# Kernel tuning notes

Measured on AMD Instinct MI355X. Metric: run time of the kernel, lower is better.

## Reference

```python
import jax, jax.numpy as jnp
import numpy as np
import math

B, S, H = 2, 4096, 512
NUM_HEADS = 8
HEAD_DIM = H // NUM_HEADS
RECENCY_DECAY = 0.9


def setup_inputs() -> dict:
    key = jax.random.key(0)
    k1, k2, k3 = jax.random.split(key, 3)
    scale = 1.0 / math.sqrt(H)
    x = jax.random.normal(k1, (B, S, H), dtype=jnp.float32)
    w_qkv = jax.random.normal(k2, (3 * H, H), dtype=jnp.float32) * scale
    w_out = jax.random.normal(k3, (H, H), dtype=jnp.float32) * scale
    b_out = jnp.zeros((H,), dtype=jnp.float32)
    return {"x": x, "w_qkv": w_qkv, "w_out": w_out, "b_out": b_out}


def reference(x, w_qkv, w_out, b_out):
    batch, seq_len, hidden = x.shape
    nh, hd = NUM_HEADS, HEAD_DIM
    # qkv projection (no bias): torch Linear computes x @ W.T
    qkv = jnp.einsum('bsh,oh->bso', x, w_qkv)
    qkv = qkv.reshape(batch, seq_len, 3, nh, hd)
    q, k, v = jnp.transpose(qkv, (2, 0, 3, 1, 4))  # each [B, nh, S, hd]
    attn = jnp.einsum('bhqd,bhkd->bhqk', q, k) / math.sqrt(hd)
    # recency bias: positions[i, j] = j - i; bias = (j-i)*log(decay) for j<=i else 0
    pos = jnp.arange(seq_len)[None, :] - jnp.arange(seq_len)[:, None]
    bias = jnp.where(pos <= 0, pos.astype(jnp.float32) * math.log(RECENCY_DECAY),
                     jnp.zeros((), dtype=jnp.float32))
    attn = jax.nn.softmax(attn + bias[None, None, :, :], axis=-1)
    out = jnp.einsum('bhqk,bhkd->bqhd', attn, v).reshape(batch, seq_len, hidden)
    return jnp.einsum('bsh,oh->bso', out, w_out) + b_out
```

## Files before the change

### kernel.cpp

```cpp
#include <hip/hip_runtime.h>
#include <hip/hip_bf16.h>
#include <hip/hip_fp16.h>
#include <stdint.h>

#define B_   2
#define S_   4096
#define H_   512
#define NH_  8
#define HD_  64
#define M_   (B_*S_)
#define LOG2D (-0.15200309344504997f)
#define SC2   (0.18033688011112042f)

#define NFULL        4
#define NCHUNK       8

typedef __attribute__((ext_vector_type(8))) short bf16x8_t;
typedef __attribute__((ext_vector_type(4))) float f32x4_t;

__device__ __forceinline__ void gl_lds16(const __hip_bfloat16* g, __hip_bfloat16* l) {
  __builtin_amdgcn_global_load_lds(
      (__attribute__((address_space(1))) void*)(g),
      (__attribute__((address_space(3))) void*)(l),
      16, 0, 0);
}

__global__ __launch_bounds__(256)
void cast3_kernel(const float* __restrict__ x, const float* __restrict__ wq,
                  const float* __restrict__ wo,
                  __hip_bfloat16* __restrict__ xb, __hip_bfloat16* __restrict__ wqb,
                  __hip_bfloat16* __restrict__ wob) {
  const int N0 = M_ * H_;
  const int N1 = 3 * H_ * H_;
  int i4 = (blockIdx.x * blockDim.x + threadIdx.x) * 4;
  const float* src; __hip_bfloat16* dst; int off;
  if (i4 < N0)           { src = x;  dst = xb;  off = i4; }
  else if (i4 < N0 + N1) { src = wq; dst = wqb; off = i4 - N0; }
  else                   { src = wo; dst = wob; off = i4 - N0 - N1; }
  float4 v = *(const float4*)(src + off);
  ushort4 o;
  __hip_bfloat16 h;
  h = __float2bfloat16(v.x); o.x = *(unsigned short*)&h;
  h = __float2bfloat16(v.y); o.y = *(unsigned short*)&h;
  h = __float2bfloat16(v.z); o.z = *(unsigned short*)&h;
  h = __float2bfloat16(v.w); o.w = *(unsigned short*)&h;
  *(ushort4*)((unsigned short*)dst + off) = o;
}

template<int EPI>
__global__ __launch_bounds__(256)
void gemm_bt(const __hip_bfloat16* __restrict__ A,
             const __hip_bfloat16* __restrict__ Bw,
             int K,
             __hip_bfloat16* __restrict__ qb,
             __hip_bfloat16* __restrict__ kb,
             __hip_bfloat16* __restrict__ vtb,
             float* __restrict__ outp,
             const float* __restrict__ bias) {
  __shared__ alignas(16) __hip_bfloat16 sA[128*64];
  __shared__ alignas(16) __hip_bfloat16 sB[128*64];
  const int tid  = threadIdx.x;
  const int wave = tid >> 6, lane = tid & 63;
  const int quad = lane >> 4, l15 = lane & 15;
  const int wr = (wave >> 1) * 64, wc = (wave & 1) * 64;

  const int nbx  = gridDim.x;
  const int flat = blockIdx.y * nbx + blockIdx.x;
  const int xcd  = flat & 7, sq = flat >> 3;
  const int rows_per_xcd = gridDim.y >> 3;
  const int by = xcd * rows_per_xcd + sq / nbx;
  const int bx = sq % nbx;
  const int m0 = by * 128, n0 = bx * 128;

  const int sub  = lane >> 3;
  const int plog = (lane & 7) ^ sub;

  f32x4_t acc[4][4] = {};

  for (int kt = 0; kt < K; kt += 64) {
    __syncthreads();
    #pragma unroll
    for (int cc = 0; cc < 4; cc++) {
      int c   = wave * 4 + cc;
      int row = c * 8 + sub;
      gl_lds16(A  + (size_t)(m0 + row) * K + kt + plog * 8, sA + c * 512);
      gl_lds16(Bw + (size_t)(n0 + row) * K + kt + plog * 8, sB + c * 512);
    }
    __syncthreads();
    #pragma unroll
    for (int kh = 0; kh < 2; kh++) {
      bf16x8_t af[4], bfr[4];
      #pragma unroll
      for (int x = 0; x < 4; x++) {
        int row = wr + x * 16 + l15;
        int pos = kh * 4 + quad;
        af[x] = *(const bf16x8_t*)(sA + row * 64 + ((pos ^ (row & 7)) << 3));
      }
      #pragma unroll
      for (int y = 0; y < 4; y++) {
        int row = wc + y * 16 + l15;
        int pos = kh * 4 + quad;
        bfr[y] = *(const bf16x8_t*)(sB + row * 64 + ((pos ^ (row & 7)) << 3));
      }
      #pragma unroll
      for (int x = 0; x < 4; x++)
        #pragma unroll
        for (int y = 0; y < 4; y++)
          acc[x][y] = __builtin_amdgcn_mfma_f32_16x16x32_bf16(af[x], bfr[y], acc[x][y], 0, 0, 0);
    }
  }

  if (EPI == 0 && (n0 >> 9) == 2) {
    #pragma unroll
    for (int x = 0; x < 4; x++) {
      int gr = m0 + wr + x * 16 + quad * 4;
      int bb = gr >> 12, sb = gr & 4095;
      #pragma unroll
      for (int y = 0; y < 4; y++) {
        int rem = (n0 - 1024) + wc + y * 16 + l15;
        int h = rem >> 6, d = rem & 63;
        ushort4 o; __hip_bfloat16 hv;
        hv = __float2bfloat16(acc[x][y][0]); o.x = *(unsigned short*)&hv;
        hv = __float2bfloat16(acc[x][y][1]); o.y = *(unsigned short*)&hv;
        hv = __float2bfloat16(acc[x][y][2]); o.z = *(unsigned short*)&hv;
        hv = __float2bfloat16(acc[x][y][3]); o.w = *(unsigned short*)&hv;
        *(ushort4*)(vtb + ((size_t)(bb * NH_ + h) * HD_ + d) * S_ + sb) = o;
      }
    }
  } else {
    #pragma unroll
    for (int x = 0; x < 4; x++) {
      #pragma unroll
      for (int y = 0; y < 4; y++) {
        #pragma unroll
        for (int r = 0; r < 4; r++) {
          int gr = m0 + wr + x*16 + quad*4 + r;
          int gc = n0 + wc + y*16 + l15;
          float v = acc[x][y][r];
          if (EPI == 0) {
            int bb = gr >> 12, s = gr & 4095;
            int t  = gc >> 9,  rem = gc & 511;
            int h  = rem >> 6, d = rem & 63;
            __hip_bfloat16 hv = __float2bfloat16(v);
            int bh = bb * NH_ + h;
            if (t == 0) qb[((size_t)bh * S_ + s) * HD_ + d] = hv;
            else        kb[((size_t)bh * S_ + s) * HD_ + d] = hv;
          } else {
            outp[(size_t)gr * H_ + gc] = v + bias[gc];
          }
        }
      }
    }
  }
}

__global__ __launch_bounds__(256)
void gemm_out64(const __hip_bfloat16* __restrict__ A,
                const __hip_bfloat16* __restrict__ Bw,
                float* __restrict__ outp,
                const float* __restrict__ bias) {
  __shared__ alignas(16) __hip_bfloat16 sA[64*64];
  __shared__ alignas(16) __hip_bfloat16 sB[128*64];
  const int tid  = threadIdx.x;
  const int wave = tid >> 6, lane = tid & 63;
  const int quad = lane >> 4, l15 = lane & 15;
  const int wr = (wave >> 1) * 32, wc = (wave & 1) * 64;

  const int flat = blockIdx.x;
  const int xcd  = flat & 7, sq = flat >> 3;
  const int by = xcd * 16 + (sq >> 2);
  const int bx = sq & 3;
  const int m0 = by * 64, n0 = bx * 128;

  const int sub  = lane >> 3;
  const int plog = (lane & 7) ^ sub;

  f32x4_t acc[2][4] = {};

  for (int kt = 0; kt < H_; kt += 64) {
    __syncthreads();
    #pragma unroll
    for (int cc = 0; cc < 6; cc++) {
      int cid = wave * 6 + cc;
      if (cid < 8) {
        int row = cid * 8 + sub;
        gl_lds16(A  + (size_t)(m0 + row) * H_ + kt + plog * 8, sA + cid * 512);
      } else {
        int row = (cid - 8) * 8 + sub;
        gl_lds16(Bw + (size_t)(n0 + row) * H_ + kt + plog * 8, sB + (cid - 8) * 512);
      }
    }
    __syncthreads();
    #pragma unroll
    for (int kh = 0; kh < 2; kh++) {
      bf16x8_t af[2], bfr[4];
      #pragma unroll
      for (int x = 0; x < 2; x++) {
        int row = wr + x * 16 + l15;
        int pos = kh * 4 + quad;
        af[x] = *(const bf16x8_t*)(sA + row * 64 + ((pos ^ (row & 7)) << 3));
      }
      #pragma unroll
      for (int y = 0; y < 4; y++) {
        int row = wc + y * 16 + l15;
        int pos = kh * 4 + quad;
        bfr[y] = *(const bf16x8_t*)(sB + row * 64 + ((pos ^ (row & 7)) << 3));
      }
      #pragma unroll
      for (int x = 0; x < 2; x++)
        #pragma unroll
        for (int y = 0; y < 4; y++)
          acc[x][y] = __builtin_amdgcn_mfma_f32_16x16x32_bf16(af[x], bfr[y], acc[x][y], 0, 0, 0);
    }
  }

  #pragma unroll
  for (int x = 0; x < 2; x++) {
    #pragma unroll
    for (int y = 0; y < 4; y++) {
      #pragma unroll
      for (int r = 0; r < 4; r++) {
        int gr = m0 + wr + x*16 + quad*4 + r;
        int gc = n0 + wc + y*16 + l15;
        outp[(size_t)gr * H_ + gc] = acc[x][y][r] + bias[gc];
      }
    }
  }
}

__device__ __forceinline__ void stage_kv(const __hip_bfloat16* __restrict__ kb,
                                         const __hip_bfloat16* __restrict__ vtb,
                                         int bh, int j0,
                                         __hip_bfloat16* dK, __hip_bfloat16* dV,
                                         int wave, int lane, int sub, int plog) {
  if (wave < 2) {
    #pragma unroll
    for (int cc = 0; cc < 4; cc++) {
      int c = wave * 4 + cc;
      gl_lds16(kb + ((size_t)bh * S_ + j0 + c * 8 + sub) * HD_ + plog * 8, dK + c * 512);
    }
  } else {
    #pragma unroll
    for (int cc = 0; cc < 4; cc++) {
      int c = (wave - 2) * 4 + cc;
      gl_lds16(vtb + ((size_t)bh * HD_ + c * 8 + sub) * S_ + j0 + plog * 8, dV + c * 512);
    }
  }
}

__global__ __launch_bounds__(256)
void attn_kernel(const __hip_bfloat16* __restrict__ qb,
                 const __hip_bfloat16* __restrict__ kb,
                 const __hip_bfloat16* __restrict__ vtb,
                 __hip_bfloat16* __restrict__ ob,
                 __half* __restrict__ pO,
                 float* __restrict__ pl) {
  __shared__ alignas(16) __hip_bfloat16 sK[2][64*64];
  __shared__ alignas(16) __hip_bfloat16 sV[2][64*64];
  __shared__ alignas(16) __hip_bfloat16 sP[4][16*64];

  const int tid  = threadIdx.x;
  const int wave = tid >> 6, lane = tid & 63;
  const int quad = lane >> 4, l15 = lane & 15;

  const int flat = blockIdx.x;
  const int xcd  = flat & 7;
  const int idx  = flat >> 3;
  const int b1   = idx / 92;
  const int w    = idx % 92;
  const int bh   = xcd + (b1 << 3);

  int q0, jt0, niter, chunk = 0;
  bool direct;
  if (w < 60) { q0 = 256 + w * 64; jt0 = 0; niter = 4; direct = true; }
  else { int t = w - 60; chunk = t & 7; q0 = (t >> 3) * 64; jt0 = chunk * 8; niter = 8; direct = false; }

  const __hip_bfloat16* qrow = qb + ((size_t)bh * S_ + q0 + wave * 16 + l15) * HD_;
  bf16x8_t aQ0 = *(const bf16x8_t*)(qrow + quad * 8);
  bf16x8_t aQ1 = *(const bf16x8_t*)(qrow + 32 + quad * 8);

  f32x4_t accO[4] = {};
  float l_r[4], negM2[4];
  const int row_i = q0 + wave * 16 + quad * 4;
  #pragma unroll
  for (int r = 0; r < 4; r++) {
    l_r[r] = 0.f;
    negM2[r] = -(17.312340f - LOG2D * (float)(row_i + r));
  }

  const int sub  = lane >> 3;
  const int plog = (lane & 7) ^ sub;
  __hip_bfloat16* sPw = &sP[wave][0];

  stage_kv(kb, vtb, bh, jt0 * 64, &sK[0][0], &sV[0][0], wave, lane, sub, plog);

  for (int it = 0; it < niter; ++it) {
    const int cur = it & 1;
    __syncthreads();
    if (it < niter - 1)
      stage_kv(kb, vtb, bh, (jt0 + it + 1) * 64,
               &sK[1 - cur][0], &sV[1 - cur][0], wave, lane, sub, plog);
    const __hip_bfloat16* cK = &sK[cur][0];
    const __hip_bfloat16* cV = &sV[cur][0];
    const int j0 = (jt0 + it) * 64;

    f32x4_t sfr[4];
    __builtin_amdgcn_s_setprio(1);
    #pragma unroll
    for (int ni = 0; ni < 4; ni++) {
      int row = ni * 16 + l15;
      f32x4_t a = {};
      bf16x8_t b0 = *(const bf16x8_t*)(cK + row * 64 + ((quad       ^ (row & 7)) << 3));
      bf16x8_t b1v = *(const bf16x8_t*)(cK + row * 64 + (((quad + 4) ^ (row & 7)) << 3));
      a = __builtin_amdgcn_mfma_f32_16x16x32_bf16(aQ0, b0, a, 0, 0, 0);
      a = __builtin_amdgcn_mfma_f32_16x16x32_bf16(aQ1, b1v, a, 0, 0, 0);
      sfr[ni] = a;
    }
    __builtin_amdgcn_s_setprio(0);

    #pragma unroll
    for (int r = 0; r < 4; r++) {
      const float d0 = (float)(j0 + l15 - (row_i + r));
      const int row = quad * 4 + r;
      float psum = 0.f;
      #pragma unroll
      for (int ni = 0; ni < 4; ni++) {
        float dij = d0 + (float)(ni * 16);
        float arg = fmaf(fminf(dij, 0.f), LOG2D, fmaf(sfr[ni][r], SC2, negM2[r]));
        float p = __builtin_amdgcn_exp2f(arg);
        psum += p;
        int col = ni * 16 + l15;
        sPw[row * 64 + (((col >> 3) ^ (row & 7)) << 3) + (col & 7)] = __float2bfloat16(p);
      }
      l_r[r] += psum;
    }
    __builtin_amdgcn_sched_barrier(0);
    __builtin_amdgcn_s_waitcnt(0xC07F);
    __builtin_amdgcn_sched_barrier(0);

    bf16x8_t aP0 = *(const bf16x8_t*)(sPw + l15 * 64 + ((quad       ^ (l15 & 7)) << 3));
    bf16x8_t aP1 = *(const bf16x8_t*)(sPw + l15 * 64 + (((quad + 4) ^ (l15 & 7)) << 3));
    __builtin_amdgcn_s_setprio(1);
    #pragma unroll
    for (int nd = 0; nd < 4; nd++) {
      int row = nd * 16 + l15;
      bf16x8_t b0 = *(const bf16x8_t*)(cV + row * 64 + ((quad       ^ (row & 7)) << 3));
      bf16x8_t b1v = *(const bf16x8_t*)(cV + row * 64 + (((quad + 4) ^ (row & 7)) << 3));
      accO[nd] = __builtin_amdgcn_mfma_f32_16x16x32_bf16(aP0, b0, accO[nd], 0, 0, 0);
      accO[nd] = __builtin_amdgcn_mfma_f32_16x16x32_bf16(aP1, b1v, accO[nd], 0, 0, 0);
    }
    __builtin_amdgcn_s_setprio(0);
    __builtin_amdgcn_sched_barrier(0);
  }

  #pragma unroll
  for (int r = 0; r < 4; r++) {
    float l = l_r[r];
    #pragma unroll
    for (int msk = 1; msk < 16; msk <<= 1) l += __shfl_xor(l, msk, 64);
    l_r[r] = l;
  }

  if (direct) {
    const int b = bh >> 3, h = bh & 7;
    #pragma unroll
    for (int r = 0; r < 4; r++) {
      float invr = 1.0f / l_r[r];
      #pragma unroll
      for (int nd = 0; nd < 4; nd++) {
        int srow = q0 + wave * 16 + quad * 4 + r;
        int col  = h * HD_ + nd * 16 + l15;
        ob[((size_t)b * S_ + srow) * H_ + col] = __float2bfloat16(accO[nd][r] * invr);
      }
    }
  } else {
    const int qt = q0 >> 6;
    size_t base = ((size_t)bh * NFULL + qt) * NCHUNK + chunk;
    __half* po = pO + base * 4096;
    #pragma unroll
    for (int nd = 0; nd < 4; nd++)
      #pragma unroll
      for (int r = 0; r < 4; r++)
        po[(wave*16 + quad*4 + r) * 64 + nd*16 + l15] = __float2half(accO[nd][r]);
    if (l15 == 0) {
      #pragma unroll
      for (int r = 0; r < 4; r++)
        pl[base * 64 + wave*16 + quad*4 + r] = l_r[r];
    }
  }
}

__global__ __launch_bounds__(256)
void combine_kernel(const __half* __restrict__ pO,
                    const float* __restrict__ pl,
                    __hip_bfloat16* __restrict__ ob) {
  const int f  = blockIdx.x;
  const int bh = blockIdx.y;
  const int tid = threadIdx.x;
  const int rr = tid >> 2, cg = (tid & 3) * 16;
  const size_t base0 = ((size_t)bh * NFULL + f) * NCHUNK;

  float L = 0.f;
  #pragma unroll
  for (int c = 0; c < NCHUNK; c++) L += pl[(base0 + c) * 64 + rr];
  const float inv = 1.0f / L;

  float o[16];
  #pragma unroll
  for (int k = 0; k < 16; k++) o[k] = 0.f;
  #pragma unroll
  for (int c = 0; c < NCHUNK; c++) {
    const __half* src = pO + (base0 + c) * 4096 + rr * 64 + cg;
    #pragma unroll
    for (int k = 0; k < 16; k++) o[k] += __half2float(src[k]);
  }
  const int b = bh >> 3, h = bh & 7, s = f * 64 + rr;
  __hip_bfloat16* dst = ob + ((size_t)b * S_ + s) * H_ + h * HD_ + cg;
  #pragma unroll
  for (int k = 0; k < 16; k++) dst[k] = __float2bfloat16(o[k] * inv);
}

extern "C" void kernel_launch(void* const* d_in, const int* in_sizes, int n_in,
                              void* d_out, int out_size, void* d_ws, size_t ws_size,
                              hipStream_t stream) {
  const float* x     = (const float*)d_in[0];
  const float* w_qkv = (const float*)d_in[1];
  const float* w_out = (const float*)d_in[2];
  const float* b_out = (const float*)d_in[3];
  float* out = (float*)d_out;

  char* ws = (char*)d_ws;
  __hip_bfloat16* xb  = (__hip_bfloat16*)(ws);
  __hip_bfloat16* wqb = (__hip_bfloat16*)(ws + (8u  << 20));
  __hip_bfloat16* wob = (__hip_bfloat16*)(ws + (10u << 20));
  __hip_bfloat16* qb  = (__hip_bfloat16*)(ws + (11u << 20));
  __hip_bfloat16* kb  = (__hip_bfloat16*)(ws + (19u << 20));
  __hip_bfloat16* vtb = (__hip_bfloat16*)(ws + (27u << 20));
  __half*         pO  = (__half*)(ws + (36u << 20));
  float*          pl  = (float*)(ws + (41u << 20));
  __hip_bfloat16* ab  = xb;

  cast3_kernel<<<dim3(5120), dim3(256), 0, stream>>>(x, w_qkv, w_out, xb, wqb, wob);
  gemm_bt<0><<<dim3(12, 64), dim3(256), 0, stream>>>(xb, wqb, H_, qb, kb, vtb, nullptr, nullptr);
  attn_kernel<<<dim3(1472), dim3(256), 0, stream>>>(qb, kb, vtb, ab, pO, pl);
  combine_kernel<<<dim3(NFULL, B_ * NH_), dim3(256), 0, stream>>>(pO, pl, ab);
  gemm_out64<<<dim3(512), dim3(256), 0, stream>>>(ab, wob, out, b_out);
}
```

Measured before the change: 134.3 us.

## Process two query tiles per block in direct attention path to reuse K/V tiles

Direct-path attention blocks now each handle two 64-row query tiles (128 rows) and share each staged K/V tile between them, which halves the number of direct blocks and the grid size. The aim is to cut repeated K/V global loads and LDS staging and to spread per-block setup over more work. The cost is more registers for the doubled accumulators and Q fragments, which may lower occupancy, plus fewer blocks to fill the GPU.

```diff
diff --git a/kernel.cpp b/kernel.cpp
--- a/kernel.cpp
+++ b/kernel.cpp
@@ -266,27 +266,37 @@
   const int flat = blockIdx.x;
   const int xcd  = flat & 7;
   const int idx  = flat >> 3;
-  const int b1   = idx / 92;
-  const int w    = idx % 92;
+  const int b1   = idx / 62;
+  const int w    = idx % 62;
   const int bh   = xcd + (b1 << 3);
 
-  int q0, jt0, niter, chunk = 0;
+  int q0, jt0, niter, chunk = 0, NQ;
   bool direct;
-  if (w < 60) { q0 = 256 + w * 64; jt0 = 0; niter = 4; direct = true; }
-  else { int t = w - 60; chunk = t & 7; q0 = (t >> 3) * 64; jt0 = chunk * 8; niter = 8; direct = false; }
-
-  const __hip_bfloat16* qrow = qb + ((size_t)bh * S_ + q0 + wave * 16 + l15) * HD_;
-  bf16x8_t aQ0 = *(const bf16x8_t*)(qrow + quad * 8);
-  bf16x8_t aQ1 = *(const bf16x8_t*)(qrow + 32 + quad * 8);
-
-  f32x4_t accO[4] = {};
-  float l_r[4], negM2[4];
+  if (w < 30) { q0 = 256 + w * 128; jt0 = 0; niter = 4; direct = true;  NQ = 2; }
+  else { int t = w - 30; chunk = t & 7; q0 = (t >> 3) * 64; jt0 = chunk * 8;
+         niter = 8; direct = false; NQ = 1; }
+
+  bf16x8_t aQ0[2], aQ1[2];
+  #pragma unroll
+  for (int qi = 0; qi < 2; qi++) {
+    if (qi < NQ) {
+      const __hip_bfloat16* qrow =
+          qb + ((size_t)bh * S_ + q0 + qi * 64 + wave * 16 + l15) * HD_;
+      aQ0[qi] = *(const bf16x8_t*)(qrow + quad * 8);
+      aQ1[qi] = *(const bf16x8_t*)(qrow + 32 + quad * 8);
+    }
+  }
+
+  f32x4_t accO[2][4] = {};
+  float l_r[2][4], negM2[2][4];
   const int row_i = q0 + wave * 16 + quad * 4;
   #pragma unroll
-  for (int r = 0; r < 4; r++) {
-    l_r[r] = 0.f;
-    negM2[r] = -(17.312340f - LOG2D * (float)(row_i + r));
-  }
+  for (int qi = 0; qi < 2; qi++)
+    #pragma unroll
+    for (int r = 0; r < 4; r++) {
+      l_r[qi][r] = 0.f;
+      negM2[qi][r] = -(17.312340f - LOG2D * (float)(row_i + qi * 64 + r));
+    }
 
   const int sub  = lane >> 3;
   const int plog = (lane & 7) ^ sub;
@@ -304,73 +314,85 @@
     const __hip_bfloat16* cV = &sV[cur][0];
     const int j0 = (jt0 + it) * 64;
 
-    f32x4_t sfr[4];
-    __builtin_amdgcn_s_setprio(1);
-    #pragma unroll
-    for (int ni = 0; ni < 4; ni++) {
-      int row = ni * 16 + l15;
-      f32x4_t a = {};
-      bf16x8_t b0 = *(const bf16x8_t*)(cK + row * 64 + ((quad       ^ (row & 7)) << 3));
-      bf16x8_t b1v = *(const bf16x8_t*)(cK + row * 64 + (((quad + 4) ^ (row & 7)) << 3));
-      a = __builtin_amdgcn_mfma_f32_16x16x32_bf16(aQ0, b0, a, 0, 0, 0);
-      a = __builtin_amdgcn_mfma_f32_16x16x32_bf16(aQ1, b1v, a, 0, 0, 0);
-      sfr[ni] = a;
-    }
-    __builtin_amdgcn_s_setprio(0);
-
+    #pragma unroll
+    for (int qi = 0; qi < 2; qi++) {
+      if (qi >= NQ) break;
+
+      f32x4_t sfr[4];
+      __builtin_amdgcn_s_setprio(1);
+      #pragma unroll
+      for (int ni = 0; ni < 4; ni++) {
+        int row = ni * 16 + l15;
+        f32x4_t a = {};
+        bf16x8_t b0 = *(const bf16x8_t*)(cK + row * 64 + ((quad       ^ (row & 7)) << 3));
+        bf16x8_t b1v = *(const bf16x8_t*)(cK + row * 64 + (((quad + 4) ^ (row & 7)) << 3));
+        a = __builtin_amdgcn_mfma_f32_16x16x32_bf16(aQ0[qi], b0, a, 0, 0, 0);
+        a = __builtin_amdgcn_mfma_f32_16x16x32_bf16(aQ1[qi], b1v, a, 0, 0, 0);
+        sfr[ni] = a;
+      }
+      __builtin_amdgcn_s_setprio(0);
+
+      #pragma unroll
+      for (int r = 0; r < 4; r++) {
+        const float d0 = (float)(j0 + l15 - (row_i + qi * 64 + r));
+        const int row = quad * 4 + r;
+        float psum = 0.f;
+        #pragma unroll
+        for (int ni = 0; ni < 4; ni++) {
+          float dij = d0 + (float)(ni * 16);
+          float arg = fmaf(fminf(dij, 0.f), LOG2D, fmaf(sfr[ni][r], SC2, negM2[qi][r]));
+          float p = __builtin_amdgcn_exp2f(arg);
+          psum += p;
+          int col = ni * 16 + l15;
+          sPw[row * 64 + (((col >> 3) ^ (row & 7)) << 3) + (col & 7)] = __float2bfloat16(p);
+        }
+        l_r[qi][r] += psum;
+      }
+      __builtin_amdgcn_sched_barrier(0);
+      __builtin_amdgcn_s_waitcnt(0xC07F);
+      __builtin_amdgcn_sched_barrier(0);
+
+      bf16x8_t aP0 = *(const bf16x8_t*)(sPw + l15 * 64 + ((quad       ^ (l15 & 7)) << 3));
+      bf16x8_t aP1 = *(const bf16x8_t*)(sPw + l15 * 64 + (((quad + 4) ^ (l15 & 7)) << 3));
+      __builtin_amdgcn_s_setprio(1);
+      #pragma unroll
+      for (int nd = 0; nd < 4; nd++) {
+        int row = nd * 16 + l15;
+        bf16x8_t b0 = *(const bf16x8_t*)(cV + row * 64 + ((quad       ^ (row & 7)) << 3));
+        bf16x8_t b1v = *(const bf16x8_t*)(cV + row * 64 + (((quad + 4) ^ (row & 7)) << 3));
+        accO[qi][nd] = __builtin_amdgcn_mfma_f32_16x16x32_bf16(aP0, b0, accO[qi][nd], 0, 0, 0);
+        accO[qi][nd] = __builtin_amdgcn_mfma_f32_16x16x32_bf16(aP1, b1v, accO[qi][nd], 0, 0, 0);
+      }
+      __builtin_amdgcn_s_setprio(0);
+      __builtin_amdgcn_sched_barrier(0);
+    }
+  }
+
+  #pragma unroll
+  for (int qi = 0; qi < 2; qi++) {
+    if (qi >= NQ) break;
     #pragma unroll
     for (int r = 0; r < 4; r++) {
-      const float d0 = (float)(j0 + l15 - (row_i + r));
-      const int row = quad * 4 + r;
-      float psum = 0.f;
-      #pragma unroll
-      for (int ni = 0; ni < 4; ni++) {
-        float dij = d0 + (float)(ni * 16);
-        float arg = fmaf(fminf(dij, 0.f), LOG2D, fmaf(sfr[ni][r], SC2, negM2[r]));
-        float p = __builtin_amdgcn_exp2f(arg);
-        psum += p;
-        int col = ni * 16 + l15;
-        sPw[row * 64 + (((col >> 3) ^ (row & 7)) << 3) + (col & 7)] = __float2bfloat16(p);
-      }
-      l_r[r] += psum;
-    }
-    __builtin_amdgcn_sched_barrier(0);
-    __builtin_amdgcn_s_waitcnt(0xC07F);
-    __builtin_amdgcn_sched_barrier(0);
-
-    bf16x8_t aP0 = *(const bf16x8_t*)(sPw + l15 * 64 + ((quad       ^ (l15 & 7)) << 3));
-    bf16x8_t aP1 = *(const bf16x8_t*)(sPw + l15 * 64 + (((quad + 4) ^ (l15 & 7)) << 3));
-    __builtin_amdgcn_s_setprio(1);
-    #pragma unroll
-    for (int nd = 0; nd < 4; nd++) {
-      int row = nd * 16 + l15;
-      bf16x8_t b0 = *(const bf16x8_t*)(cV + row * 64 + ((quad       ^ (row & 7)) << 3));
-      bf16x8_t b1v = *(const bf16x8_t*)(cV + row * 64 + (((quad + 4) ^ (row & 7)) << 3));
-      accO[nd] = __builtin_amdgcn_mfma_f32_16x16x32_bf16(aP0, b0, accO[nd], 0, 0, 0);
-      accO[nd] = __builtin_amdgcn_mfma_f32_16x16x32_bf16(aP1, b1v, accO[nd], 0, 0, 0);
-    }
-    __builtin_amdgcn_s_setprio(0);
-    __builtin_amdgcn_sched_barrier(0);
-  }
-
-  #pragma unroll
-  for (int r = 0; r < 4; r++) {
-    float l = l_r[r];
-    #pragma unroll
-    for (int msk = 1; msk < 16; msk <<= 1) l += __shfl_xor(l, msk, 64);
-    l_r[r] = l;
+      float l = l_r[qi][r];
+      #pragma unroll
+      for (int msk = 1; msk < 16; msk <<= 1) l += __shfl_xor(l, msk, 64);
+      l_r[qi][r] = l;
+    }
   }
 
   if (direct) {
     const int b = bh >> 3, h = bh & 7;
     #pragma unroll
-    for (int r = 0; r < 4; r++) {
-      float invr = 1.0f / l_r[r];
-      #pragma unroll
-      for (int nd = 0; nd < 4; nd++) {
-        int srow = q0 + wave * 16 + quad * 4 + r;
-        int col  = h * HD_ + nd * 16 + l15;
-        ob[((size_t)b * S_ + srow) * H_ + col] = __float2bfloat16(accO[nd][r] * invr);
+    for (int qi = 0; qi < 2; qi++) {
+      #pragma unroll
+      for (int r = 0; r < 4; r++) {
+        float invr = 1.0f / l_r[qi][r];
+        #pragma unroll
+        for (int nd = 0; nd < 4; nd++) {
+          int srow = q0 + qi * 64 + wave * 16 + quad * 4 + r;
+          int col  = h * HD_ + nd * 16 + l15;
+          ob[((size_t)b * S_ + srow) * H_ + col] = __float2bfloat16(accO[qi][nd][r] * invr);
+        }
       }
     }
   } else {
@@ -381,11 +403,11 @@
     for (int nd = 0; nd < 4; nd++)
       #pragma unroll
       for (int r = 0; r < 4; r++)
-        po[(wave*16 + quad*4 + r) * 64 + nd*16 + l15] = __float2half(accO[nd][r]);
+        po[(wave*16 + quad*4 + r) * 64 + nd*16 + l15] = __float2half(accO[0][nd][r]);
     if (l15 == 0) {
       #pragma unroll
       for (int r = 0; r < 4; r++)
-        pl[base * 64 + wave*16 + quad*4 + r] = l_r[r];
+        pl[base * 64 + wave*16 + quad*4 + r] = l_r[0][r];
     }
   }
 }
@@ -442,7 +464,7 @@
 
   cast3_kernel<<<dim3(5120), dim3(256), 0, stream>>>(x, w_qkv, w_out, xb, wqb, wob);
   gemm_bt<0><<<dim3(12, 64), dim3(256), 0, stream>>>(xb, wqb, H_, qb, kb, vtb, nullptr, nullptr);
-  attn_kernel<<<dim3(1472), dim3(256), 0, stream>>>(qb, kb, vtb, ab, pO, pl);
+  attn_kernel<<<dim3(992), dim3(256), 0, stream>>>(qb, kb, vtb, ab, pO, pl);
   combine_kernel<<<dim3(NFULL, B_ * NH_), dim3(256), 0, stream>>>(pO, pl, ab);
   gemm_out64<<<dim3(512), dim3(256), 0, stream>>>(ab, wob, out, b_out);
 }
```

Result: no change. 132.4 us (median of 2 runs) (-1.5%).
